# Kernel tuning notes

Hardware: AMD Instinct MI355X
Metric: run time of the kernel (lower is better)

The kernel has to match this reference:

```python
import jax, jax.numpy as jnp
import numpy as np

B, C, H, W = 8, 256, 48, 48
C8 = C // 8


def _conv1x1(w, b, t):
    # w: [O, C], b: [O], t: [B, C, H, W] -> [B, O, H, W]
    return jnp.einsum('oc,bchw->bohw', w, t) + b[None, :, None, None]


def setup_inputs() -> dict:
    key = jax.random.key(0)
    ks = jax.random.split(key, 16)
    s_qk = 1.0 / np.sqrt(C)
    inp = {
        'x': jax.random.normal(ks[0], (B, C, H, W), jnp.float32),
        'y': jax.random.normal(ks[1], (B, C, H, W), jnp.float32),
        'wqx': jax.random.normal(ks[2], (C8, C), jnp.float32) * s_qk,
        'bqx': jax.random.normal(ks[3], (C8,), jnp.float32) * 0.01,
        'wkx': jax.random.normal(ks[4], (C8, C), jnp.float32) * s_qk,
        'bkx': jax.random.normal(ks[5], (C8,), jnp.float32) * 0.01,
        'wvx': jax.random.normal(ks[6], (C, C), jnp.float32) * s_qk,
        'bvx': jax.random.normal(ks[7], (C,), jnp.float32) * 0.01,
        'wqy': jax.random.normal(ks[8], (C8, C), jnp.float32) * s_qk,
        'bqy': jax.random.normal(ks[9], (C8,), jnp.float32) * 0.01,
        'wky': jax.random.normal(ks[10], (C8, C), jnp.float32) * s_qk,
        'bky': jax.random.normal(ks[11], (C8,), jnp.float32) * 0.01,
        'wvy': jax.random.normal(ks[12], (C, C), jnp.float32) * s_qk,
        'bvy': jax.random.normal(ks[13], (C,), jnp.float32) * 0.01,
        'gamma_x': jax.random.normal(ks[14], (1,), jnp.float32) * 0.1,
        'gamma_y': jax.random.normal(ks[15], (1,), jnp.float32) * 0.1,
    }
    return inp


def reference(x, y, wqx, bqx, wkx, bkx, wvx, bvx, wqy, bqy, wky, bky, wvy, bvy, gamma_x, gamma_y):
    b, c, h, w = x.shape
    n = h * w
    # x-branch projections, flattened to [B, ch, N]
    q1 = _conv1x1(wqx, bqx, x).reshape(b, -1, n)  # [B, C8, N]
    k1 = _conv1x1(wkx, bkx, x).reshape(b, -1, n)
    v1 = _conv1x1(wvx, bvx, x).reshape(b, -1, n)  # [B, C, N]
    # y-branch
    q2 = _conv1x1(wqy, bqy, y).reshape(b, -1, n)
    k2 = _conv1x1(wky, bky, y).reshape(b, -1, n)
    v2 = _conv1x1(wvy, bvy, y).reshape(b, -1, n)
    # energy[b,i,j] = sum_c q[b,c,i]*k[b,c,j]; softmax over j (no 1/sqrt(d) scaling)
    attn1 = jax.nn.softmax(jnp.einsum('bci,bcj->bij', q1, k1), axis=-1)  # [B, N, N]
    attn2 = jax.nn.softmax(jnp.einsum('bci,bcj->bij', q2, k2), axis=-1)
    # cross value routing: out1 uses v1 with attn2^T, out2 uses v2 with attn1^T
    out1 = jnp.einsum('bcj,bij->bci', v1, attn2).reshape(b, c, h, w)
    out2 = jnp.einsum('bcj,bij->bci', v2, attn1).reshape(b, c, h, w)
    out1 = gamma_x * out1 + x
    out2 = gamma_y * out2 + y
    return (out1, out2)
```

## Files before the change

kernel.cpp:

```cpp
#include <hip/hip_runtime.h>
#include <math.h>

#define BB 8
#define CC 256
#define CQ 32
#define NN 2304
#define NT 36
#define NJ 36

typedef __attribute__((ext_vector_type(8))) short bf16x8;
typedef __attribute__((ext_vector_type(4))) float f32x4;
typedef __attribute__((ext_vector_type(4))) unsigned short u16x4;
typedef unsigned short ushort_t;
typedef unsigned int u32;

#define LOG2E 1.44269504088896f

static __device__ inline unsigned short f2bf(float f) {
    unsigned u = __builtin_bit_cast(unsigned, f);
    return (unsigned short)((u + 0x7fffu + ((u >> 16) & 1u)) >> 16);
}

static __device__ inline void gld_lds16(const ushort_t* g, ushort_t* l) {
    __builtin_amdgcn_global_load_lds(
        (const __attribute__((address_space(1))) u32*)g,
        (__attribute__((address_space(3))) u32*)l, 16, 0, 0);
}

#define S8  ((size_t)BB * NN * CQ)
#define SV  ((size_t)BB * NN * CC)
#define WOFF (4 * S8 + 2 * SV)

__global__ __launch_bounds__(256) void wcvt_kernel(
    const float* __restrict__ wqx, const float* __restrict__ bqx,
    const float* __restrict__ wkx, const float* __restrict__ bkx,
    const float* __restrict__ wvx, const float* __restrict__ bvx,
    const float* __restrict__ wqy, const float* __restrict__ bqy,
    const float* __restrict__ wky, const float* __restrict__ bky,
    const float* __restrict__ wvy, const float* __restrict__ bvy,
    ushort_t* __restrict__ ws)
{
    ushort_t* Wall = ws + WOFF;
    float*    ball = (float*)(ws + WOFF + 2 * 320 * 256);

    int id = blockIdx.x * 256 + threadIdx.x;
    int row = id >> 6;
    int c4  = (id & 63) * 4;
    int br  = row >= 320;
    int r   = row - br * 320;

    const float* src;
    float scale = 1.0f;
    if (r < 32)      { src = (br ? wqy : wqx) + (size_t)r * CC;        scale = LOG2E; }
    else if (r < 64) { src = (br ? wky : wkx) + (size_t)(r - 32) * CC; }
    else             { src = (br ? wvy : wvx) + (size_t)(r - 64) * CC; }

    float4 v = *(const float4*)(src + c4);
    u16x4 pk;
    pk[0] = f2bf(v.x * scale); pk[1] = f2bf(v.y * scale);
    pk[2] = f2bf(v.z * scale); pk[3] = f2bf(v.w * scale);
    *(u16x4*)(Wall + (size_t)row * CC + c4) = pk;

    if (id < 640) {
        int row2 = id, br2 = row2 >= 320, r2 = row2 - br2 * 320;
        const float* bsrc; float sc2 = 1.0f;
        if (r2 < 32)      { bsrc = (br2 ? bqy : bqx) + r2;        sc2 = LOG2E; }
        else if (r2 < 64) { bsrc = (br2 ? bky : bkx) + (r2 - 32); }
        else              { bsrc = (br2 ? bvy : bvx) + (r2 - 64); }
        ball[row2] = bsrc[0] * sc2;
    }
}

__global__ __launch_bounds__(256, 2) void proj_kernel(
    const float* __restrict__ x, const float* __restrict__ y,
    ushort_t* __restrict__ ws)
{
    __shared__ __align__(16) ushort_t vls[256 * 64];

    const int t = threadIdx.x, w = t >> 6, lane = t & 63;
    const int l15 = lane & 15, quad = lane >> 4;

    const int id   = blockIdx.x;
    const int b    = id & 7;
    const int rest = id >> 3;
    const int br   = rest >= NT;
    const int tile = br ? rest - NT : rest;

    const float* src = br ? y : x;
    const ushort_t* Wall = ws + WOFF + (size_t)br * 320 * CC;
    const float*    ball = (float*)(ws + WOFF + 2 * 320 * 256) + br * 320;

    ushort_t* qbuf = ws + (size_t)br * 2 * S8;
    ushort_t* kbuf = qbuf + S8;
    ushort_t* vbufg = ws + 4 * S8 + (size_t)br * SV;

    const int px0 = tile * 64 + w * 16;

    const float* ap = src + (size_t)b * CC * NN + px0 + l15;
    bf16x8 af[8];
#pragma unroll
    for (int q = 0; q < 8; q++) {
        float av[8];
#pragma unroll
        for (int j = 0; j < 8; j++)
            av[j] = ap[(size_t)(q * 32 + quad * 8 + j) * NN];
        union { bf16x8 v; unsigned short u[8]; } tmp;
#pragma unroll
        for (int j = 0; j < 8; j++) tmp.u[j] = f2bf(av[j]);
        af[q] = tmp.v;
    }

    const ushort_t* wb = Wall + (size_t)l15 * CC + quad * 8;
    f32x4 acc[20];
#pragma unroll
    for (int ot = 0; ot < 20; ot++) {
        f32x4 a = (f32x4){0.f, 0.f, 0.f, 0.f};
#pragma unroll
        for (int q = 0; q < 8; q++)
            a = __builtin_amdgcn_mfma_f32_16x16x32_bf16(
                    af[q], *(const bf16x8*)(wb + (size_t)(ot * 16) * CC + q * 32),
                    a, 0, 0, 0);
        acc[ot] = a;
    }

#pragma unroll
    for (int ot = 0; ot < 4; ot++) {
        int o = ot * 16 + l15;
        float bias = ball[o];
        ushort_t* dst = (o < 32 ? qbuf : kbuf);
        int oc = o & 31;
#pragma unroll
        for (int r = 0; r < 4; r++) {
            int pxl = w * 16 + quad * 4 + r;
            dst[((size_t)b * NN + tile * 64 + pxl) * CQ + oc] = f2bf(acc[ot][r] + bias);
        }
    }
#pragma unroll
    for (int ot = 4; ot < 20; ot++) {
        int o_loc = (ot - 4) * 16 + l15;
        float bias = ball[64 + o_loc];
#pragma unroll
        for (int r = 0; r < 4; r++) {
            int pxl = w * 16 + quad * 4 + r;
            vls[o_loc * 64 + (((pxl >> 3) ^ (o_loc & 7)) * 8) + (pxl & 7)] =
                f2bf(acc[ot][r] + bias);
        }
    }
    __syncthreads();
#pragma unroll
    for (int rep = 0; rep < 8; rep++) {
        int cid = rep * 256 + t;
        int o_loc = cid >> 3, pc = cid & 7;
        *(uint4*)(vbufg + ((size_t)b * CC + o_loc) * NN + tile * 64 + pc * 8) =
            *(uint4*)&vls[cid * 8];
    }
}

#define TI 64
#define TJ 64

__global__ __launch_bounds__(256, 2) void flash_kernel(
    const float* __restrict__ x, const float* __restrict__ y,
    const float* __restrict__ gxp, const float* __restrict__ gyp,
    const ushort_t* __restrict__ ws, float* __restrict__ out)
{
    __shared__ __align__(16) ushort_t Vs[2][256 * 64];
    __shared__ __align__(16) ushort_t Ps[2][64 * 64];
    float* Lrow = (float*)&Ps[0][0];
    float* Ob   = (float*)&Vs[0][0];

    const int t = threadIdx.x, w = t >> 6, lane = t & 63;
    const int l15 = lane & 15, quad = lane >> 4;

    const int id   = blockIdx.x;
    const int b    = id & 7;
    const int rest = id >> 3;
    const int br   = rest >= NT;
    const int it   = br ? rest - NT : rest;
    const int i0   = it * TI;

    const ushort_t* Qb = ws + (br ? 0 : 2 * S8);
    const ushort_t* Kb = Qb + S8;
    const ushort_t* Vb = ws + 4 * S8 + (br ? SV : 0);
    const float* res = br ? y : x;
    const float gamma = br ? gyp[0] : gxp[0];
    float* op = out + (size_t)br * SV + (size_t)b * CC * NN;

    bf16x8 qf = *(const bf16x8*)(Qb + ((size_t)b * NN + i0 + w * 16 + l15) * CQ + quad * 8);

    f32x4 acc[4][4];
#pragma unroll
    for (int i = 0; i < 4; i++)
#pragma unroll
        for (int j = 0; j < 4; j++) acc[i][j] = (f32x4){0.f, 0.f, 0.f, 0.f};
    float l_loc[4] = {0.f, 0.f, 0.f, 0.f};

    const ushort_t* Vg = Vb + (size_t)b * CC * NN
                       + (size_t)(w * 64 + (lane >> 3)) * NN + (lane & 7) * 8;
    const ushort_t* kp = Kb + ((size_t)b * NN + l15) * CQ + quad * 8;

    {
        ushort_t* l = &Vs[0][(w * 64) * 64];
#pragma unroll
        for (int is = 0; is < 8; is++)
            gld_lds16(Vg + (size_t)is * 8 * NN, l + is * 512);
    }
    bf16x8 kfA[4], kfB[4];
#pragma unroll
    for (int n = 0; n < 4; n++)
        kfA[n] = *(const bf16x8*)(kp + (size_t)(n * 16) * CQ);
#pragma unroll
    for (int n = 0; n < 4; n++)
        kfB[n] = *(const bf16x8*)(kp + (size_t)(TJ + n * 16) * CQ);

    f32x4 sP[4];
#pragma unroll
    for (int n = 0; n < 4; n++)
        sP[n] = __builtin_amdgcn_mfma_f32_16x16x32_bf16(
                    qf, kfA[n], (f32x4){0.f, 0.f, 0.f, 0.f}, 0, 0, 0);

#define FLASH_ITER(JT, CUR, KFQK, KFLD)                                         \
    {                                                                           \
          \
        if ((JT) + 1 < NJ) {                                                    \
            ushort_t* l = &Vs[(CUR) ^ 1][(w * 64) * 64];                        \
            const ushort_t* g = Vg + (size_t)((JT) + 1) * TJ;                   \
            _Pragma("unroll")                                                   \
            for (int is = 0; is < 8; is++)                                      \
                gld_lds16(g + (size_t)is * 8 * NN, l + is * 512);               \
        }                                                                       \
                \
        if ((JT) + 2 < NJ) {                                                    \
            const ushort_t* kn = kp + (size_t)(((JT) + 2) * TJ) * CQ;           \
            _Pragma("unroll")                                                   \
            for (int n = 0; n < 4; n++)                                         \
                KFLD[n] = *(const bf16x8*)(kn + (size_t)(n * 16) * CQ);         \
        }                                                                       \
                   \
        unsigned short pu[4][4];                                                \
        _Pragma("unroll")                                                       \
        for (int n = 0; n < 4; n++)                                             \
            _Pragma("unroll")                                                   \
            for (int r = 0; r < 4; r++) {                                       \
                float p = __builtin_amdgcn_exp2f(sP[n][r]);                     \
                l_loc[r] += p;                                                  \
                pu[n][r] = f2bf(p);                                             \
            }                                                                   \
            \
        _Pragma("unroll")                                                       \
        for (int n = 0; n < 4; n++)                                             \
            _Pragma("unroll")                                                   \
            for (int r = 0; r < 4; r++) {                                       \
                int row = w * 16 + quad * 4 + r;                                \
                int ch  = (n * 2 + (l15 >> 3)) ^ (row & 7);                     \
                Ps[CUR][row * 64 + ch * 8 + (l15 & 7)] = pu[n][r];              \
            }                                                                   \
                    \
        if ((JT) + 1 < NJ) {                                                    \
            _Pragma("unroll")                                                   \
            for (int n = 0; n < 4; n++)                                         \
                sP[n] = __builtin_amdgcn_mfma_f32_16x16x32_bf16(                \
                    qf, KFQK[n], (f32x4){0.f, 0.f, 0.f, 0.f}, 0, 0, 0);         \
        }                                                                       \
                  \
        asm volatile("s_waitcnt lgkmcnt(0)" ::: "memory");                      \
        __builtin_amdgcn_s_barrier();                                           \
         \
        if ((JT) + 2 < NJ) asm volatile("s_waitcnt vmcnt(12)" ::: "memory");    \
        else               asm volatile("s_waitcnt vmcnt(0)"  ::: "memory");    \
                                       \
        _Pragma("unroll")                                                       \
        for (int ks = 0; ks < 2; ks++) {                                        \
            bf16x8 pf[4], vf[4];                                                \
            _Pragma("unroll")                                                   \
            for (int rt = 0; rt < 4; rt++) {                                    \
                int prow = rt * 16 + l15;                                       \
                int pch  = (ks * 4 + quad) ^ (l15 & 7);                         \
                pf[rt] = *(const bf16x8*)&Ps[CUR][prow * 64 + pch * 8];         \
            }                                                                   \
            _Pragma("unroll")                                                   \
            for (int ct = 0; ct < 4; ct++) {                                    \
                int row = w * 64 + ct * 16 + l15;                               \
                int pc  = (ks * 4 + quad) ^ (l15 & 7);                          \
                vf[ct] = *(const bf16x8*)&Vs[CUR][row * 64 + pc * 8];           \
            }                                                                   \
            __builtin_amdgcn_s_setprio(1);                                      \
            _Pragma("unroll")                                                   \
            for (int rt = 0; rt < 4; rt++)                                      \
                _Pragma("unroll")                                               \
                for (int ct = 0; ct < 4; ct++)                                  \
                    acc[rt][ct] = __builtin_amdgcn_mfma_f32_16x16x32_bf16(      \
                        pf[rt], vf[ct], acc[rt][ct], 0, 0, 0);                  \
            __builtin_amdgcn_s_setprio(0);                                      \
        }                                                                       \
    }

    for (int jt = 0; jt < NJ; jt += 2) {
        FLASH_ITER(jt,     0, kfB, kfA)
        FLASH_ITER(jt + 1, 1, kfA, kfB)
    }
#undef FLASH_ITER

#pragma unroll
    for (int r = 0; r < 4; r++) {
        float l = l_loc[r];
        l += __shfl_xor(l, 1);
        l += __shfl_xor(l, 2);
        l += __shfl_xor(l, 4);
        l += __shfl_xor(l, 8);
        l_loc[r] = l;
    }
    if (l15 == 0) {
        f32x4 lv = {l_loc[0], l_loc[1], l_loc[2], l_loc[3]};
        *(f32x4*)&Lrow[w * 16 + quad * 4] = lv;
    }
    __syncthreads();

    for (int rt = 0; rt < 4; rt++) {
        f32x4 lv = *(f32x4*)&Lrow[rt * 16 + quad * 4];
        f32x4 gi;
#pragma unroll
        for (int r = 0; r < 4; r++) gi[r] = gamma / lv[r];
#pragma unroll
        for (int ct = 0; ct < 4; ct++) {
            int c = w * 64 + ct * 16 + l15;
            f32x4 ov;
#pragma unroll
            for (int r = 0; r < 4; r++) ov[r] = acc[rt][ct][r] * gi[r];
            *(f32x4*)&Ob[c * 20 + quad * 4] = ov;
        }
        __syncthreads();
#pragma unroll
        for (int rep = 0; rep < 4; rep++) {
            int c  = rep * 64 + (t >> 2);
            int p4 = t & 3;
            f32x4 v = *(f32x4*)&Ob[c * 20 + p4 * 4];
            size_t go = ((size_t)b * CC + c) * NN + i0 + rt * 16 + p4 * 4;
            f32x4 r4 = *(const f32x4*)&res[go];
            v += r4;
            *(f32x4*)&op[(size_t)c * NN + i0 + rt * 16 + p4 * 4] = v;
        }
        __syncthreads();
    }
}

extern "C" void kernel_launch(void* const* d_in, const int* in_sizes, int n_in,
                              void* d_out, int out_size, void* d_ws, size_t ws_size,
                              hipStream_t stream)
{
    const float* x   = (const float*)d_in[0];
    const float* y   = (const float*)d_in[1];
    const float* wqx = (const float*)d_in[2];
    const float* bqx = (const float*)d_in[3];
    const float* wkx = (const float*)d_in[4];
    const float* bkx = (const float*)d_in[5];
    const float* wvx = (const float*)d_in[6];
    const float* bvx = (const float*)d_in[7];
    const float* wqy = (const float*)d_in[8];
    const float* bqy = (const float*)d_in[9];
    const float* wky = (const float*)d_in[10];
    const float* bky = (const float*)d_in[11];
    const float* wvy = (const float*)d_in[12];
    const float* bvy = (const float*)d_in[13];
    const float* gx  = (const float*)d_in[14];
    const float* gy  = (const float*)d_in[15];
    ushort_t* ws = (ushort_t*)d_ws;
    float* out = (float*)d_out;

    wcvt_kernel<<<dim3(160), 256, 0, stream>>>(wqx, bqx, wkx, bkx, wvx, bvx,
                                               wqy, bqy, wky, bky, wvy, bvy, ws);
    proj_kernel<<<dim3(576), 256, 0, stream>>>(x, y, ws);
    flash_kernel<<<dim3(576), 256, 0, stream>>>(x, y, gx, gy, ws, out);
}
```

Baseline: 258.7 us.

## Load V fragments directly into registers and drop LDS staging in flash kernel

The flash kernel no longer stages V tiles through double-buffered LDS with global_load_lds. Each wave now loads its own V MFMA operands straight from global memory into double-buffered register arrays that are prefetched one tile ahead. The epilogue writes gamma-scaled output plus residual directly from the accumulators, removing the LDS transpose and its barriers. The projection kernel's V staging uses a padded row stride instead of an XOR swizzle. This cuts LDS footprint and LDS traffic, which may allow higher occupancy, but it adds register pressure and less coalesced, strided global loads and stores.

```diff
diff --git a/kernel.cpp b/kernel.cpp
--- a/kernel.cpp
+++ b/kernel.cpp
@@ -19,12 +19,6 @@
 static __device__ inline unsigned short f2bf(float f) {
     unsigned u = __builtin_bit_cast(unsigned, f);
     return (unsigned short)((u + 0x7fffu + ((u >> 16) & 1u)) >> 16);
-}
-
-static __device__ inline void gld_lds16(const ushort_t* g, ushort_t* l) {
-    __builtin_amdgcn_global_load_lds(
-        (const __attribute__((address_space(1))) u32*)g,
-        (__attribute__((address_space(3))) u32*)l, 16, 0, 0);
 }
 
 #define S8  ((size_t)BB * NN * CQ)
@@ -75,7 +69,7 @@
     const float* __restrict__ x, const float* __restrict__ y,
     ushort_t* __restrict__ ws)
 {
-    __shared__ __align__(16) ushort_t vls[256 * 64];
+    __shared__ __align__(16) ushort_t vls[256 * 68];
 
     const int t = threadIdx.x, w = t >> 6, lane = t & 63;
     const int l15 = lane & 15, quad = lane >> 4;
@@ -142,8 +136,7 @@
 #pragma unroll
         for (int r = 0; r < 4; r++) {
             int pxl = w * 16 + quad * 4 + r;
-            vls[o_loc * 64 + (((pxl >> 3) ^ (o_loc & 7)) * 8) + (pxl & 7)] =
-                f2bf(acc[ot][r] + bias);
+            vls[o_loc * 68 + pxl] = f2bf(acc[ot][r] + bias);
         }
     }
     __syncthreads();
@@ -152,7 +145,7 @@
         int cid = rep * 256 + t;
         int o_loc = cid >> 3, pc = cid & 7;
         *(uint4*)(vbufg + ((size_t)b * CC + o_loc) * NN + tile * 64 + pc * 8) =
-            *(uint4*)&vls[cid * 8];
+            *(uint4*)&vls[o_loc * 68 + pc * 8];
     }
 }
 
@@ -164,10 +157,8 @@
     const float* __restrict__ gxp, const float* __restrict__ gyp,
     const ushort_t* __restrict__ ws, float* __restrict__ out)
 {
-    __shared__ __align__(16) ushort_t Vs[2][256 * 64];
     __shared__ __align__(16) ushort_t Ps[2][64 * 64];
-    float* Lrow = (float*)&Ps[0][0];
-    float* Ob   = (float*)&Vs[0][0];
+    __shared__ __align__(16) float Lrow[64];
 
     const int t = threadIdx.x, w = t >> 6, lane = t & 63;
     const int l15 = lane & 15, quad = lane >> 4;
@@ -196,15 +187,21 @@
     float l_loc[4] = {0.f, 0.f, 0.f, 0.f};
 
     const ushort_t* Vg = Vb + (size_t)b * CC * NN
-                       + (size_t)(w * 64 + (lane >> 3)) * NN + (lane & 7) * 8;
+                       + (size_t)(w * 64 + l15) * NN + quad * 8;
     const ushort_t* kp = Kb + ((size_t)b * NN + l15) * CQ + quad * 8;
 
-    {
-        ushort_t* l = &Vs[0][(w * 64) * 64];
-#pragma unroll
-        for (int is = 0; is < 8; is++)
-            gld_lds16(Vg + (size_t)is * 8 * NN, l + is * 512);
-    }
+#define LOAD_VF(DST, T)                                                         \
+    {                                                                           \
+        _Pragma("unroll")                                                       \
+        for (int ct = 0; ct < 4; ct++)                                          \
+            _Pragma("unroll")                                                   \
+            for (int ks = 0; ks < 2; ks++)                                      \
+                DST[ks * 4 + ct] = *(const bf16x8*)(Vg                          \
+                    + (size_t)(ct * 16) * NN + (size_t)(T) * TJ + ks * 32);     \
+    }
+
+    bf16x8 vfA[8], vfB[8];
+    LOAD_VF(vfA, 0)
     bf16x8 kfA[4], kfB[4];
 #pragma unroll
     for (int n = 0; n < 4; n++)
@@ -219,17 +216,10 @@
         sP[n] = __builtin_amdgcn_mfma_f32_16x16x32_bf16(
                     qf, kfA[n], (f32x4){0.f, 0.f, 0.f, 0.f}, 0, 0, 0);
 
-#define FLASH_ITER(JT, CUR, KFQK, KFLD)                                         \
+#define FLASH_ITER(JT, CUR, KFQK, KFLD, VFC, VFN)                               \
     {                                                                           \
-          \
-        if ((JT) + 1 < NJ) {                                                    \
-            ushort_t* l = &Vs[(CUR) ^ 1][(w * 64) * 64];                        \
-            const ushort_t* g = Vg + (size_t)((JT) + 1) * TJ;                   \
-            _Pragma("unroll")                                                   \
-            for (int is = 0; is < 8; is++)                                      \
-                gld_lds16(g + (size_t)is * 8 * NN, l + is * 512);               \
-        }                                                                       \
-                \
+           \
+        if ((JT) + 1 < NJ) LOAD_VF(VFN, (JT) + 1)                               \
         if ((JT) + 2 < NJ) {                                                    \
             const ushort_t* kn = kp + (size_t)(((JT) + 2) * TJ) * CQ;           \
             _Pragma("unroll")                                                   \
@@ -265,41 +255,34 @@
                   \
         asm volatile("s_waitcnt lgkmcnt(0)" ::: "memory");                      \
         __builtin_amdgcn_s_barrier();                                           \
-         \
-        if ((JT) + 2 < NJ) asm volatile("s_waitcnt vmcnt(12)" ::: "memory");    \
-        else               asm volatile("s_waitcnt vmcnt(0)"  ::: "memory");    \
-                                       \
+              \
+                      \
         _Pragma("unroll")                                                       \
         for (int ks = 0; ks < 2; ks++) {                                        \
-            bf16x8 pf[4], vf[4];                                                \
+            bf16x8 pf[4];                                                       \
             _Pragma("unroll")                                                   \
             for (int rt = 0; rt < 4; rt++) {                                    \
                 int prow = rt * 16 + l15;                                       \
                 int pch  = (ks * 4 + quad) ^ (l15 & 7);                         \
                 pf[rt] = *(const bf16x8*)&Ps[CUR][prow * 64 + pch * 8];         \
             }                                                                   \
-            _Pragma("unroll")                                                   \
-            for (int ct = 0; ct < 4; ct++) {                                    \
-                int row = w * 64 + ct * 16 + l15;                               \
-                int pc  = (ks * 4 + quad) ^ (l15 & 7);                          \
-                vf[ct] = *(const bf16x8*)&Vs[CUR][row * 64 + pc * 8];           \
-            }                                                                   \
             __builtin_amdgcn_s_setprio(1);                                      \
             _Pragma("unroll")                                                   \
             for (int rt = 0; rt < 4; rt++)                                      \
                 _Pragma("unroll")                                               \
                 for (int ct = 0; ct < 4; ct++)                                  \
                     acc[rt][ct] = __builtin_amdgcn_mfma_f32_16x16x32_bf16(      \
-                        pf[rt], vf[ct], acc[rt][ct], 0, 0, 0);                  \
+                        pf[rt], VFC[ks * 4 + ct], acc[rt][ct], 0, 0, 0);        \
             __builtin_amdgcn_s_setprio(0);                                      \
         }                                                                       \
     }
 
     for (int jt = 0; jt < NJ; jt += 2) {
-        FLASH_ITER(jt,     0, kfB, kfA)
-        FLASH_ITER(jt + 1, 1, kfA, kfB)
+        FLASH_ITER(jt,     0, kfB, kfA, vfA, vfB)
+        FLASH_ITER(jt + 1, 1, kfA, kfB, vfB, vfA)
     }
 #undef FLASH_ITER
+#undef LOAD_VF
 
 #pragma unroll
     for (int r = 0; r < 4; r++) {
@@ -316,6 +299,7 @@
     }
     __syncthreads();
 
+#pragma unroll
     for (int rt = 0; rt < 4; rt++) {
         f32x4 lv = *(f32x4*)&Lrow[rt * 16 + quad * 4];
         f32x4 gi;
@@ -324,23 +308,13 @@
 #pragma unroll
         for (int ct = 0; ct < 4; ct++) {
             int c = w * 64 + ct * 16 + l15;
+            size_t off = (size_t)c * NN + i0 + rt * 16 + quad * 4;
+            f32x4 r4 = *(const f32x4*)&res[(size_t)b * CC * NN + off];
             f32x4 ov;
 #pragma unroll
-            for (int r = 0; r < 4; r++) ov[r] = acc[rt][ct][r] * gi[r];
-            *(f32x4*)&Ob[c * 20 + quad * 4] = ov;
+            for (int r = 0; r < 4; r++) ov[r] = acc[rt][ct][r] * gi[r] + r4[r];
+            *(f32x4*)&op[off] = ov;
         }
-        __syncthreads();
-#pragma unroll
-        for (int rep = 0; rep < 4; rep++) {
-            int c  = rep * 64 + (t >> 2);
-            int p4 = t & 3;
-            f32x4 v = *(f32x4*)&Ob[c * 20 + p4 * 4];
-            size_t go = ((size_t)b * CC + c) * NN + i0 + rt * 16 + p4 * 4;
-            f32x4 r4 = *(const f32x4*)&res[go];
-            v += r4;
-            *(f32x4*)&op[(size_t)c * NN + i0 + rt * 16 + p4 * 4] = v;
-        }
-        __syncthreads();
     }
 }
 
```

Result: slower. 375.1 us (+45.0%).

## Stage projection weights through double-buffered LDS with swizzled layout

Applied to the files above, without the earlier changes.

The projection kernel now copies the bf16 weight matrix into LDS in five 64-row chunks using global_load_lds, double-buffered so the next chunk loads while MFMAs run on the current one. Previously every wave read its weight fragments directly from global memory. The weight-prep kernel writes weights in an XOR-swizzled column order so the LDS fragment reads avoid bank conflicts. LDS use grows from 32KB to 64KB per block, and the old V staging buffer is reused as scratch. The extra barriers per chunk and the higher LDS footprint may limit occupancy.

```diff
diff --git a/kernel.cpp b/kernel.cpp
--- a/kernel.cpp
+++ b/kernel.cpp
@@ -59,7 +59,10 @@
     u16x4 pk;
     pk[0] = f2bf(v.x * scale); pk[1] = f2bf(v.y * scale);
     pk[2] = f2bf(v.z * scale); pk[3] = f2bf(v.w * scale);
-    *(u16x4*)(Wall + (size_t)row * CC + c4) = pk;
+    int ch16 = c4 >> 3;
+    int half = (c4 >> 2) & 1;
+    int dcol = (((ch16 ^ (row & 7)) << 3) + (half << 2));
+    *(u16x4*)(Wall + (size_t)row * CC + dcol) = pk;
 
     if (id < 640) {
         int row2 = id, br2 = row2 >= 320, r2 = row2 - br2 * 320;
@@ -75,7 +78,7 @@
     const float* __restrict__ x, const float* __restrict__ y,
     ushort_t* __restrict__ ws)
 {
-    __shared__ __align__(16) ushort_t vls[256 * 64];
+    __shared__ __align__(16) ushort_t Wls[2][64 * 256];
 
     const int t = threadIdx.x, w = t >> 6, lane = t & 63;
     const int l15 = lane & 15, quad = lane >> 4;
@@ -96,6 +99,17 @@
 
     const int px0 = tile * 64 + w * 16;
 
+#define STAGE_W(CH, BUF)                                                        \
+    {                                                                           \
+        const ushort_t* g = Wall + (size_t)(CH) * (64 * CC);                    \
+        _Pragma("unroll")                                                       \
+        for (int i = 0; i < 8; i++)                                             \
+            gld_lds16(g + (size_t)(i * 256 + w * 64 + lane) * 8,                \
+                      &Wls[BUF][(i * 256 + w * 64) * 8]);                       \
+    }
+
+    STAGE_W(0, 0)
+
     const float* ap = src + (size_t)b * CC * NN + px0 + l15;
     bf16x8 af[8];
 #pragma unroll
@@ -110,19 +124,47 @@
         af[q] = tmp.v;
     }
 
-    const ushort_t* wb = Wall + (size_t)l15 * CC + quad * 8;
     f32x4 acc[20];
-#pragma unroll
-    for (int ot = 0; ot < 20; ot++) {
-        f32x4 a = (f32x4){0.f, 0.f, 0.f, 0.f};
-#pragma unroll
-        for (int q = 0; q < 8; q++)
-            a = __builtin_amdgcn_mfma_f32_16x16x32_bf16(
-                    af[q], *(const bf16x8*)(wb + (size_t)(ot * 16) * CC + q * 32),
-                    a, 0, 0, 0);
-        acc[ot] = a;
-    }
-
+    const int rx = l15 & 7;
+
+#define PROJ_CHUNK(CH, BUF)                                                     \
+    {                                                                           \
+        if ((CH) + 1 < 5) STAGE_W((CH) + 1, ((CH) + 1) & 1)                     \
+        if ((CH) + 1 < 5) asm volatile("s_waitcnt vmcnt(8)" ::: "memory");      \
+        else              asm volatile("s_waitcnt vmcnt(0)" ::: "memory");      \
+        __builtin_amdgcn_s_barrier();                                           \
+        const ushort_t* w0 = &Wls[BUF][(size_t)(0 * 16 + l15) * 256];           \
+        const ushort_t* w1 = &Wls[BUF][(size_t)(1 * 16 + l15) * 256];           \
+        const ushort_t* w2 = &Wls[BUF][(size_t)(2 * 16 + l15) * 256];           \
+        const ushort_t* w3 = &Wls[BUF][(size_t)(3 * 16 + l15) * 256];           \
+        f32x4 a0 = (f32x4){0.f, 0.f, 0.f, 0.f};                                 \
+        f32x4 a1 = a0, a2 = a0, a3 = a0;                                        \
+        _Pragma("unroll")                                                       \
+        for (int q = 0; q < 8; q++) {                                           \
+            int co = ((q * 4 + quad) ^ rx) << 3;                                \
+            bf16x8 b0 = *(const bf16x8*)(w0 + co);                              \
+            bf16x8 b1 = *(const bf16x8*)(w1 + co);                              \
+            bf16x8 b2 = *(const bf16x8*)(w2 + co);                              \
+            bf16x8 b3 = *(const bf16x8*)(w3 + co);                              \
+            a0 = __builtin_amdgcn_mfma_f32_16x16x32_bf16(af[q], b0, a0, 0,0,0); \
+            a1 = __builtin_amdgcn_mfma_f32_16x16x32_bf16(af[q], b1, a1, 0,0,0); \
+            a2 = __builtin_amdgcn_mfma_f32_16x16x32_bf16(af[q], b2, a2, 0,0,0); \
+            a3 = __builtin_amdgcn_mfma_f32_16x16x32_bf16(af[q], b3, a3, 0,0,0); \
+        }                                                                       \
+        acc[(CH) * 4 + 0] = a0; acc[(CH) * 4 + 1] = a1;                         \
+        acc[(CH) * 4 + 2] = a2; acc[(CH) * 4 + 3] = a3;                         \
+        __builtin_amdgcn_s_barrier();                                           \
+    }
+
+    PROJ_CHUNK(0, 0)
+    PROJ_CHUNK(1, 1)
+    PROJ_CHUNK(2, 0)
+    PROJ_CHUNK(3, 1)
+    PROJ_CHUNK(4, 0)
+#undef PROJ_CHUNK
+#undef STAGE_W
+
+    ushort_t* scratch = &Wls[0][0];
 #pragma unroll
     for (int ot = 0; ot < 4; ot++) {
         int o = ot * 16 + l15;
@@ -142,7 +184,7 @@
 #pragma unroll
         for (int r = 0; r < 4; r++) {
             int pxl = w * 16 + quad * 4 + r;
-            vls[o_loc * 64 + (((pxl >> 3) ^ (o_loc & 7)) * 8) + (pxl & 7)] =
+            scratch[o_loc * 64 + (((pxl >> 3) ^ (o_loc & 7)) * 8) + (pxl & 7)] =
                 f2bf(acc[ot][r] + bias);
         }
     }
@@ -152,7 +194,7 @@
         int cid = rep * 256 + t;
         int o_loc = cid >> 3, pc = cid & 7;
         *(uint4*)(vbufg + ((size_t)b * CC + o_loc) * NN + tile * 64 + pc * 8) =
-            *(uint4*)&vls[cid * 8];
+            *(uint4*)&scratch[cid * 8];
     }
 }
 
@@ -268,7 +310,7 @@
          \
         if ((JT) + 2 < NJ) asm volatile("s_waitcnt vmcnt(12)" ::: "memory");    \
         else               asm volatile("s_waitcnt vmcnt(0)"  ::: "memory");    \
-                                       \
+                                            \
         _Pragma("unroll")                                                       \
         for (int ks = 0; ks < 2; ks++) {                                        \
             bf16x8 pf[4], vf[4];                                                \
```

Result: faster. 216.7 us (-16.2%).
